# Optimization experiments

Hardware: AMD Instinct MI355X
Metric: run time of the kernel (lower is better)

Reference implementation:

```python
import jax, jax.numpy as jnp
import numpy as np

N_NODES = 50000
NEG_SLOPE = 0.2  # PyG GATConv leaky_relu default


def _gat_layer(x, src, dst, W, a_src, a_dst, bias, heads, ch):
    n = x.shape[0]
    h = (x @ W).reshape(n, heads, ch)                    # [N,H,C]
    alpha_s = jnp.sum(h * a_src, axis=-1)                # [N,H]
    alpha_d = jnp.sum(h * a_dst, axis=-1)                # [N,H]
    e = alpha_s[src] + alpha_d[dst]                      # [E,H]
    e = jnp.where(e > 0, e, NEG_SLOPE * e)               # leaky_relu
    # segment softmax over incoming edges of each dst node
    m = jax.ops.segment_max(e, dst, num_segments=n)      # [N,H]
    m = jnp.where(jnp.isfinite(m), m, 0.0)
    ex = jnp.exp(e - m[dst])                             # [E,H]
    denom = jax.ops.segment_sum(ex, dst, num_segments=n) # [N,H]
    alpha = ex / (denom[dst] + 1e-16)                    # [E,H]
    msg = alpha[:, :, None] * h[src]                     # [E,H,C]
    out = jax.ops.segment_sum(msg, dst, num_segments=n)  # [N,H,C]
    return out.reshape(n, heads * ch) + bias


def setup_inputs() -> dict:
    key = jax.random.key(0)
    ks = jax.random.split(key, 10)
    F_in, H1, C1, C2 = 256, 8, 32, 32
    E = 500000
    x = jax.random.normal(ks[0], (N_NODES, F_in), dtype=jnp.float32)
    edge_index = jax.random.randint(ks[1], (2, E), 0, N_NODES, dtype=jnp.int64)
    s1 = 1.0 / np.sqrt(F_in)
    s2 = 1.0 / np.sqrt(H1 * C1)
    return {
        "x": x,
        "edge_index": edge_index,
        "W1": jax.random.normal(ks[2], (F_in, H1 * C1), dtype=jnp.float32) * s1,
        "a_src1": jax.random.normal(ks[3], (H1, C1), dtype=jnp.float32) * s2,
        "a_dst1": jax.random.normal(ks[4], (H1, C1), dtype=jnp.float32) * s2,
        "b1": jnp.zeros((H1 * C1,), dtype=jnp.float32),
        "W2": jax.random.normal(ks[5], (H1 * C1, C2), dtype=jnp.float32) * s2,
        "a_src2": jax.random.normal(ks[6], (1, C2), dtype=jnp.float32) * (1.0 / np.sqrt(C2)),
        "a_dst2": jax.random.normal(ks[7], (1, C2), dtype=jnp.float32) * (1.0 / np.sqrt(C2)),
        "b2": jnp.zeros((C2,), dtype=jnp.float32),
    }


def reference(x, edge_index, W1, a_src1, a_dst1, b1, W2, a_src2, a_dst2, b2):
    n = x.shape[0]
    # add self-loops (PyG GATConv default add_self_loops=True)
    loop = jnp.arange(n, dtype=edge_index.dtype)
    src = jnp.concatenate([edge_index[0], loop])
    dst = jnp.concatenate([edge_index[1], loop])
    h = _gat_layer(x, src, dst, W1, a_src1, a_dst1, b1, heads=8, ch=32)
    h = jax.nn.elu(h)
    h = _gat_layer(h, src, dst, W2, a_src2, a_dst2, b2, heads=1, ch=32)
    return jax.nn.log_softmax(h, axis=1)
```

## Files before the change

### kernel.cpp

```cpp
#include <hip/hip_runtime.h>
#include <math.h>


typedef __attribute__((ext_vector_type(8))) short bf16x8;
typedef __attribute__((ext_vector_type(4))) float f32x4;

__device__ __forceinline__ float bf2f(ushort u) {
    union { uint i; float f; } v; v.i = ((uint)u) << 16; return v.f;
}
__device__ __forceinline__ ushort f2bf(float f) {
    union { float f; uint i; } v; v.f = f;
    uint r = v.i + 0x7FFFu + ((v.i >> 16) & 1u);
    return (ushort)(r >> 16);
}

__global__ void zero_kernel(int* p, int n) {
    int i = blockIdx.x * blockDim.x + threadIdx.x;
    if (i < n) p[i] = 0;
}

__global__ void detect_kernel(const int* ei32, int* flag) {
    __shared__ int cnt;
    if (threadIdx.x == 0) cnt = 0;
    __syncthreads();
    int nz = 0;
    for (int i = threadIdx.x; i < 1024; i += blockDim.x)
        if (ei32[2 * i + 1] != 0) nz++;
    atomicAdd(&cnt, nz);
    __syncthreads();
    if (threadIdx.x == 0) *flag = (cnt > 16) ? 1 : 0;
}

__global__ void decode_degree_kernel(const void* ei, int E, int ET, int N,
                                     const int* __restrict__ flag,
                                     int* __restrict__ src, int* __restrict__ dst,
                                     int* __restrict__ deg) {
    int k = blockIdx.x * blockDim.x + threadIdx.x;
    if (k >= ET) return;
    int s, d;
    if (k < E) {
        if (*flag) {
            const int* p = (const int*)ei;
            s = p[k]; d = p[E + k];
        } else {
            const long long* p = (const long long*)ei;
            s = (int)p[k]; d = (int)p[E + k];
        }
    } else {
        s = d = k - E;
    }
    s = min(max(s, 0), N - 1);
    d = min(max(d, 0), N - 1);
    src[k] = s; dst[k] = d;
    atomicAdd(&deg[d], 1);
}

__global__ __launch_bounds__(256) void scanA_kernel(const int* __restrict__ deg,
                                                    int* __restrict__ bsum, int n) {
    int i = blockIdx.x * 256 + threadIdx.x;
    int v = (i < n) ? deg[i] : 0;
#pragma unroll
    for (int s = 1; s < 64; s <<= 1) v += __shfl_xor(v, s, 64);
    __shared__ int ws[4];
    int lane = threadIdx.x & 63, wid = threadIdx.x >> 6;
    if (lane == 0) ws[wid] = v;
    __syncthreads();
    if (threadIdx.x == 0) bsum[blockIdx.x] = ws[0] + ws[1] + ws[2] + ws[3];
}

__global__ __launch_bounds__(1024) void scanB_kernel(int* __restrict__ bsum, int nb) {
    int t = threadIdx.x;
    int v = (t < nb) ? bsum[t] : 0;
    __shared__ int sm[1024];
    sm[t] = v;
    __syncthreads();
    for (int s = 1; s < 1024; s <<= 1) {
        int a = (t >= s) ? sm[t - s] : 0;
        __syncthreads();
        sm[t] += a;
        __syncthreads();
    }
    if (t < nb) bsum[t] = sm[t] - v;
}

__global__ __launch_bounds__(256) void scanC_kernel(const int* __restrict__ deg,
                                                    const int* __restrict__ bsum,
                                                    int* __restrict__ off, int n) {
    int t = threadIdx.x;
    int i = blockIdx.x * 256 + t;
    int v = (i < n) ? deg[i] : 0;
    int incl = v;
    int lane = t & 63, wid = t >> 6;
#pragma unroll
    for (int s = 1; s < 64; s <<= 1) {
        int a = __shfl_up(incl, s, 64);
        if (lane >= s) incl += a;
    }
    __shared__ int wsum[4];
    if (lane == 63) wsum[wid] = incl;
    __syncthreads();
    int wo = 0;
    for (int w = 0; w < wid; w++) wo += wsum[w];
    if (i < n) off[i + 1] = bsum[blockIdx.x] + wo + incl;
    if (i == 0) off[0] = 0;
}

__global__ void scatter_kernel(const int* __restrict__ src, const int* __restrict__ dst,
                               int ET, const int* __restrict__ off,
                               int* __restrict__ cursor, int* __restrict__ esrc) {
    int k = blockIdx.x * blockDim.x + threadIdx.x;
    if (k >= ET) return;
    int d = dst[k];
    int p = atomicAdd(&cursor[d], 1);
    esrc[off[d] + p] = src[k];
}

__global__ void convert_x(const float* __restrict__ x, ushort* __restrict__ xb, long n) {
    long i = ((long)blockIdx.x * blockDim.x + threadIdx.x) * 8;
    if (i >= n) return;
    float4 a = *(const float4*)&x[i];
    float4 b = *(const float4*)&x[i + 4];
    uint4 o;
    o.x = (uint)f2bf(a.x) | ((uint)f2bf(a.y) << 16);
    o.y = (uint)f2bf(a.z) | ((uint)f2bf(a.w) << 16);
    o.z = (uint)f2bf(b.x) | ((uint)f2bf(b.y) << 16);
    o.w = (uint)f2bf(b.z) | ((uint)f2bf(b.w) << 16);
    *(uint4*)&xb[i] = o;
}

__global__ __launch_bounds__(256) void convert_w1t(const float* __restrict__ W1,
                                                   ushort* __restrict__ w1t) {
    __shared__ float tile[32][33];
    int tx = threadIdx.x & 31, ty = threadIdx.x >> 5;
    int bx = blockIdx.x, by = blockIdx.y;
    for (int i = 0; i < 32; i += 8)
        tile[ty + i][tx] = W1[(by * 32 + ty + i) * 256 + bx * 32 + tx];
    __syncthreads();
    for (int i = 0; i < 32; i += 8)
        w1t[(bx * 32 + ty + i) * 256 + by * 32 + tx] = f2bf(tile[tx][ty + i]);
}

__global__ __launch_bounds__(256) void convert_w2t(const float* __restrict__ W2,
                                                   ushort* __restrict__ w2t) {
    int idx = blockIdx.x * 256 + threadIdx.x;
    int c = idx >> 8, k = idx & 255;
    w2t[idx] = f2bf(W2[k * 32 + c]);
}

#define LDA 72
__global__ __launch_bounds__(256) void gemm1_mfma(
        const ushort* __restrict__ xb,
        const ushort* __restrict__ w1t,
        ushort* __restrict__ h1b,
        int N) {
    __shared__ ushort Al[128 * LDA];
    __shared__ ushort Bl[128 * LDA];
    int t = threadIdx.x;
    int row0 = blockIdx.x * 128;
    int n0 = blockIdx.y * 128;
    int lane = t & 63, wid = t >> 6;
    int wr = wid >> 1, wc = wid & 1;

    f32x4 acc[4][4] = {};

    int sr = t >> 1, scs = (t & 1) * 32;
    for (int k0 = 0; k0 < 256; k0 += 64) {
        {
            int gr = row0 + sr;
            uint4 v0 = {0,0,0,0}, v1 = {0,0,0,0}, v2 = {0,0,0,0}, v3 = {0,0,0,0};
            if (gr < N) {
                const uint4* g = (const uint4*)(xb + (size_t)gr * 256 + k0 + scs);
                v0 = g[0]; v1 = g[1]; v2 = g[2]; v3 = g[3];
            }
            uint4* d = (uint4*)&Al[sr * LDA + scs];
            d[0] = v0; d[1] = v1; d[2] = v2; d[3] = v3;
        }
        {
            const uint4* g = (const uint4*)(w1t + (size_t)(n0 + sr) * 256 + k0 + scs);
            uint4* d = (uint4*)&Bl[sr * LDA + scs];
            d[0] = g[0]; d[1] = g[1]; d[2] = g[2]; d[3] = g[3];
        }
        __syncthreads();

#pragma unroll
        for (int ks = 0; ks < 2; ks++) {
            int kk = ks * 32 + (lane >> 4) * 8;
            bf16x8 af[4], bfr[4];
#pragma unroll
            for (int mi = 0; mi < 4; mi++) {
                int r = wr * 64 + mi * 16 + (lane & 15);
                af[mi] = *(const bf16x8*)&Al[r * LDA + kk];
            }
#pragma unroll
            for (int ni = 0; ni < 4; ni++) {
                int r = wc * 64 + ni * 16 + (lane & 15);
                bfr[ni] = *(const bf16x8*)&Bl[r * LDA + kk];
            }
#pragma unroll
            for (int mi = 0; mi < 4; mi++)
#pragma unroll
                for (int ni = 0; ni < 4; ni++)
                    acc[mi][ni] = __builtin_amdgcn_mfma_f32_16x16x32_bf16(
                        af[mi], bfr[ni], acc[mi][ni], 0, 0, 0);
        }
        __syncthreads();
    }

#pragma unroll
    for (int mi = 0; mi < 4; mi++)
#pragma unroll
        for (int ni = 0; ni < 4; ni++) {
            int gc = n0 + wc * 64 + ni * 16 + (lane & 15);
#pragma unroll
            for (int j = 0; j < 4; j++) {
                int gr = row0 + wr * 64 + mi * 16 + (lane >> 4) * 4 + j;
                if (gr < N) h1b[(size_t)gr * 256 + gc] = f2bf(acc[mi][ni][j]);
            }
        }
}

__global__ __launch_bounds__(256) void alpha1_kernel(
        const ushort* __restrict__ h1b,
        const float* __restrict__ a_src1, const float* __restrict__ a_dst1,
        float* __restrict__ as1, float* __restrict__ ad1, int N) {
    int t = threadIdx.x;
    int g = t >> 5, l = t & 31;
    int node = blockIdx.x * 8 + g;
    if (node >= N) return;
    bf16x8 hv = *(const bf16x8*)&h1b[(size_t)node * 256 + l * 8];
    float s = 0.f, d = 0.f;
#pragma unroll
    for (int i = 0; i < 8; i++) {
        float h = bf2f((ushort)hv[i]);
        s = fmaf(h, a_src1[l * 8 + i], s);
        d = fmaf(h, a_dst1[l * 8 + i], d);
    }
    s += __shfl_xor(s, 1); s += __shfl_xor(s, 2);
    d += __shfl_xor(d, 1); d += __shfl_xor(d, 2);
    if ((l & 3) == 0) {
        as1[node * 8 + (l >> 2)] = s;
        ad1[node * 8 + (l >> 2)] = d;
    }
}

__global__ __launch_bounds__(256) void weights1_kernel(
        const float* __restrict__ as1, const float* __restrict__ ad1,
        const int* __restrict__ off, const int* __restrict__ esrc,
        float* __restrict__ alf1, int NH) {
    int tid = blockIdx.x * 256 + threadIdx.x;
    if (tid >= NH) return;
    int node = tid >> 3, head = tid & 7;
    int beg = off[node], end = off[node + 1];
    float adv = ad1[tid];
    float m = -3.0e38f;
    for (int j = beg; j < end; j++) {
        float e = as1[esrc[j] * 8 + head] + adv;
        e = (e > 0.f) ? e : 0.2f * e;
        m = fmaxf(m, e);
    }
    float dnm = 0.f;
    for (int j = beg; j < end; j++) {
        float e = as1[esrc[j] * 8 + head] + adv;
        e = (e > 0.f) ? e : 0.2f * e;
        dnm += __expf(e - m);
    }
    float inv = 1.f / (dnm + 1e-16f);
    for (int j = beg; j < end; j++) {
        float e = as1[esrc[j] * 8 + head] + adv;
        e = (e > 0.f) ? e : 0.2f * e;
        alf1[(size_t)j * 8 + head] = __expf(e - m) * inv;
    }
}

__global__ __launch_bounds__(256) void agg1b_kernel(
        const ushort* __restrict__ h1b, const float* __restrict__ alf1,
        const float* __restrict__ b1,
        const int* __restrict__ off, const int* __restrict__ esrc,
        ushort* __restrict__ hactb, int N) {
    int t = threadIdx.x;
    int node = blockIdx.x * 4 + (t >> 6);
    int lane = t & 63;
    if (node >= N) return;
    int beg = off[node], end = off[node + 1];
    int ch0 = lane * 4;
    int head = lane >> 3;
    const ushort* hb = h1b + ch0;
    const float* af = alf1 + head;
    float c0 = 0.f, c1 = 0.f, c2 = 0.f, c3 = 0.f;
    int j = beg;
    for (; j + 4 <= end; j += 4) {
        int s0 = esrc[j + 0], s1 = esrc[j + 1], s2 = esrc[j + 2], s3 = esrc[j + 3];
        float w0 = af[(size_t)(j + 0) * 8];
        float w1 = af[(size_t)(j + 1) * 8];
        float w2 = af[(size_t)(j + 2) * 8];
        float w3 = af[(size_t)(j + 3) * 8];
        uint2 v0 = *(const uint2*)(hb + (size_t)s0 * 256);
        uint2 v1 = *(const uint2*)(hb + (size_t)s1 * 256);
        uint2 v2 = *(const uint2*)(hb + (size_t)s2 * 256);
        uint2 v3 = *(const uint2*)(hb + (size_t)s3 * 256);
        c0 = fmaf(w0, bf2f((ushort)(v0.x & 0xffffu)), c0);
        c1 = fmaf(w0, bf2f((ushort)(v0.x >> 16)), c1);
        c2 = fmaf(w0, bf2f((ushort)(v0.y & 0xffffu)), c2);
        c3 = fmaf(w0, bf2f((ushort)(v0.y >> 16)), c3);
        c0 = fmaf(w1, bf2f((ushort)(v1.x & 0xffffu)), c0);
        c1 = fmaf(w1, bf2f((ushort)(v1.x >> 16)), c1);
        c2 = fmaf(w1, bf2f((ushort)(v1.y & 0xffffu)), c2);
        c3 = fmaf(w1, bf2f((ushort)(v1.y >> 16)), c3);
        c0 = fmaf(w2, bf2f((ushort)(v2.x & 0xffffu)), c0);
        c1 = fmaf(w2, bf2f((ushort)(v2.x >> 16)), c1);
        c2 = fmaf(w2, bf2f((ushort)(v2.y & 0xffffu)), c2);
        c3 = fmaf(w2, bf2f((ushort)(v2.y >> 16)), c3);
        c0 = fmaf(w3, bf2f((ushort)(v3.x & 0xffffu)), c0);
        c1 = fmaf(w3, bf2f((ushort)(v3.x >> 16)), c1);
        c2 = fmaf(w3, bf2f((ushort)(v3.y & 0xffffu)), c2);
        c3 = fmaf(w3, bf2f((ushort)(v3.y >> 16)), c3);
    }
    for (; j < end; j++) {
        int s0 = esrc[j];
        float w = af[(size_t)j * 8];
        uint2 v = *(const uint2*)(hb + (size_t)s0 * 256);
        c0 = fmaf(w, bf2f((ushort)(v.x & 0xffffu)), c0);
        c1 = fmaf(w, bf2f((ushort)(v.x >> 16)), c1);
        c2 = fmaf(w, bf2f((ushort)(v.y & 0xffffu)), c2);
        c3 = fmaf(w, bf2f((ushort)(v.y >> 16)), c3);
    }
    float4 bv = *(const float4*)&b1[ch0];
    float o0 = c0 + bv.x, o1 = c1 + bv.y, o2 = c2 + bv.z, o3 = c3 + bv.w;
    o0 = (o0 > 0.f) ? o0 : (__expf(o0) - 1.f);
    o1 = (o1 > 0.f) ? o1 : (__expf(o1) - 1.f);
    o2 = (o2 > 0.f) ? o2 : (__expf(o2) - 1.f);
    o3 = (o3 > 0.f) ? o3 : (__expf(o3) - 1.f);
    uint2 r;
    r.x = (uint)f2bf(o0) | ((uint)f2bf(o1) << 16);
    r.y = (uint)f2bf(o2) | ((uint)f2bf(o3) << 16);
    *(uint2*)(hactb + (size_t)node * 256 + ch0) = r;
}

__global__ __launch_bounds__(256) void gemm2_mfma(
        const ushort* __restrict__ hactb,
        const ushort* __restrict__ w2t,
        float* __restrict__ h2, int N) {
    __shared__ ushort Al[128 * LDA];
    __shared__ ushort Bl[32 * LDA];
    int t = threadIdx.x;
    int row0 = blockIdx.x * 128;
    int lane = t & 63, wid = t >> 6;

    f32x4 acc[2][2] = {};

    int sr = t >> 1, scs = (t & 1) * 32;
    for (int k0 = 0; k0 < 256; k0 += 64) {
        {
            int gr = row0 + sr;
            uint4 v0 = {0,0,0,0}, v1 = {0,0,0,0}, v2 = {0,0,0,0}, v3 = {0,0,0,0};
            if (gr < N) {
                const uint4* g = (const uint4*)(hactb + (size_t)gr * 256 + k0 + scs);
                v0 = g[0]; v1 = g[1]; v2 = g[2]; v3 = g[3];
            }
            uint4* d = (uint4*)&Al[sr * LDA + scs];
            d[0] = v0; d[1] = v1; d[2] = v2; d[3] = v3;
        }
        if (t < 64) {
            const uint4* g = (const uint4*)(w2t + (size_t)sr * 256 + k0 + scs);
            uint4* d = (uint4*)&Bl[sr * LDA + scs];
            d[0] = g[0]; d[1] = g[1]; d[2] = g[2]; d[3] = g[3];
        }
        __syncthreads();

#pragma unroll
        for (int ks = 0; ks < 2; ks++) {
            int kk = ks * 32 + (lane >> 4) * 8;
            bf16x8 af[2], bfr[2];
#pragma unroll
            for (int mi = 0; mi < 2; mi++) {
                int r = wid * 32 + mi * 16 + (lane & 15);
                af[mi] = *(const bf16x8*)&Al[r * LDA + kk];
            }
#pragma unroll
            for (int ni = 0; ni < 2; ni++) {
                int r = ni * 16 + (lane & 15);
                bfr[ni] = *(const bf16x8*)&Bl[r * LDA + kk];
            }
#pragma unroll
            for (int mi = 0; mi < 2; mi++)
#pragma unroll
                for (int ni = 0; ni < 2; ni++)
                    acc[mi][ni] = __builtin_amdgcn_mfma_f32_16x16x32_bf16(
                        af[mi], bfr[ni], acc[mi][ni], 0, 0, 0);
        }
        __syncthreads();
    }

#pragma unroll
    for (int mi = 0; mi < 2; mi++)
#pragma unroll
        for (int ni = 0; ni < 2; ni++) {
            int gc = ni * 16 + (lane & 15);
#pragma unroll
            for (int j = 0; j < 4; j++) {
                int gr = row0 + wid * 32 + mi * 16 + (lane >> 4) * 4 + j;
                if (gr < N) h2[(size_t)gr * 32 + gc] = acc[mi][ni][j];
            }
        }
}

__global__ __launch_bounds__(256) void alpha2_kernel(
        const float* __restrict__ h2,
        const float* __restrict__ a_src2, const float* __restrict__ a_dst2,
        float* __restrict__ as2, float* __restrict__ ad2, int N) {
    int t = threadIdx.x;
    int g = t >> 3, q = t & 7;
    int node = blockIdx.x * 32 + g;
    if (node >= N) return;
    float4 v = *(const float4*)&h2[(size_t)node * 32 + q * 4];
    float4 sa = *(const float4*)&a_src2[q * 4];
    float4 da = *(const float4*)&a_dst2[q * 4];
    float s = v.x * sa.x + v.y * sa.y + v.z * sa.z + v.w * sa.w;
    float d = v.x * da.x + v.y * da.y + v.z * da.z + v.w * da.w;
    s += __shfl_xor(s, 1, 8); s += __shfl_xor(s, 2, 8); s += __shfl_xor(s, 4, 8);
    d += __shfl_xor(d, 1, 8); d += __shfl_xor(d, 2, 8); d += __shfl_xor(d, 4, 8);
    if (q == 0) { as2[node] = s; ad2[node] = d; }
}

__global__ __launch_bounds__(256) void weights2_kernel(
        const float* __restrict__ as2, const float* __restrict__ ad2,
        const int* __restrict__ off, const int* __restrict__ esrc,
        float* __restrict__ alf2, int N) {
    int t = threadIdx.x;
    int g = t >> 5, lane = t & 31;
    int node = blockIdx.x * 8 + g;
    if (node >= N) return;
    int beg = off[node], end = off[node + 1];
    float adv = ad2[node];
    float m = -3.0e38f, dnm = 0.f;
    for (int base = beg; base < end; base += 32) {
        int n_ch = min(32, end - base);
        float ej = -3.0e38f;
        if (lane < n_ch) {
            float e = as2[esrc[base + lane]] + adv;
            ej = (e > 0.f) ? e : 0.2f * e;
        }
        float cm = ej;
#pragma unroll
        for (int s = 16; s > 0; s >>= 1) cm = fmaxf(cm, __shfl_xor(cm, s, 32));
        float nm = fmaxf(m, cm);
        float scl = __expf(m - nm);
        float wj = (lane < n_ch) ? __expf(ej - nm) : 0.f;
        float ws = wj;
#pragma unroll
        for (int s = 16; s > 0; s >>= 1) ws += __shfl_xor(ws, s, 32);
        dnm = dnm * scl + ws;
        m = nm;
    }
    float inv = 1.f / (dnm + 1e-16f);
    for (int base = beg; base < end; base += 32) {
        int n_ch = min(32, end - base);
        if (lane < n_ch) {
            float e = as2[esrc[base + lane]] + adv;
            e = (e > 0.f) ? e : 0.2f * e;
            alf2[base + lane] = __expf(e - m) * inv;
        }
    }
}

__global__ __launch_bounds__(256) void agg2b_kernel(
        const float* __restrict__ h2, const float* __restrict__ alf2,
        const float* __restrict__ b2,
        const int* __restrict__ off, const int* __restrict__ esrc,
        float* __restrict__ out, int N) {
    int t = threadIdx.x;
    int g = t >> 5, c = t & 31;
    int node = blockIdx.x * 8 + g;
    if (node >= N) return;
    int beg = off[node], end = off[node + 1];
    const float* hcol = h2 + c;
    float a0 = 0.f, a1 = 0.f, a2 = 0.f, a3 = 0.f;
    int j = beg;
    for (; j + 4 <= end; j += 4) {
        int s0 = esrc[j + 0], s1 = esrc[j + 1], s2 = esrc[j + 2], s3 = esrc[j + 3];
        float w0 = alf2[j + 0], w1 = alf2[j + 1], w2 = alf2[j + 2], w3 = alf2[j + 3];
        a0 = fmaf(w0, hcol[(size_t)s0 * 32], a0);
        a1 = fmaf(w1, hcol[(size_t)s1 * 32], a1);
        a2 = fmaf(w2, hcol[(size_t)s2 * 32], a2);
        a3 = fmaf(w3, hcol[(size_t)s3 * 32], a3);
    }
    for (; j < end; j++)
        a0 = fmaf(alf2[j], hcol[(size_t)esrc[j] * 32], a0);
    float v = (a0 + a1) + (a2 + a3) + b2[c];
    float mx = v;
#pragma unroll
    for (int s = 16; s > 0; s >>= 1) mx = fmaxf(mx, __shfl_xor(mx, s, 32));
    float sum = __expf(v - mx);
#pragma unroll
    for (int s = 16; s > 0; s >>= 1) sum += __shfl_xor(sum, s, 32);
    out[(size_t)node * 32 + c] = (v - mx) - __logf(sum);
}

extern "C" void kernel_launch(void* const* d_in, const int* in_sizes, int n_in,
                              void* d_out, int out_size, void* d_ws, size_t ws_size,
                              hipStream_t stream) {
    const float* x      = (const float*)d_in[0];
    const void*  ei     = d_in[1];
    const float* W1     = (const float*)d_in[2];
    const float* a_src1 = (const float*)d_in[3];
    const float* a_dst1 = (const float*)d_in[4];
    const float* b1     = (const float*)d_in[5];
    const float* W2     = (const float*)d_in[6];
    const float* a_src2 = (const float*)d_in[7];
    const float* a_dst2 = (const float*)d_in[8];
    const float* b2     = (const float*)d_in[9];
    const int N  = in_sizes[0] / 256;
    const int E  = in_sizes[1] / 2;
    const int ET = E + N;
    float* outp = (float*)d_out;
    (void)n_in; (void)out_size; (void)ws_size;

    char* ws = (char*)d_ws;
    size_t o = 0;
    auto alloc = [&](size_t bytes) -> void* {
        void* p = ws + o;
        o += (bytes + 255) & ~(size_t)255;
        return p;
    };
    int*    flag   = (int*)alloc(4);
    int*    src32  = (int*)alloc((size_t)ET * 4);
    int*    dst32  = (int*)alloc((size_t)ET * 4);
    int*    deg    = (int*)alloc((size_t)2 * N * 4);
    int*    cursor = deg + N;
    int*    off    = (int*)alloc((size_t)(N + 1) * 4);
    int*    esrc   = (int*)alloc((size_t)ET * 4);
    int*    bsum   = (int*)alloc((size_t)1024 * 4);
    ushort* xb     = (ushort*)alloc((size_t)N * 256 * 2);
    ushort* w1t    = (ushort*)alloc((size_t)256 * 256 * 2);
    ushort* w2t    = (ushort*)alloc((size_t)32 * 256 * 2);
    ushort* h1b    = (ushort*)alloc((size_t)N * 256 * 2);
    float*  as1    = (float*)alloc((size_t)N * 8 * 4);
    float*  ad1    = (float*)alloc((size_t)N * 8 * 4);
    float*  alf1   = (float*)alloc((size_t)ET * 8 * 4);
    ushort* hactb  = (ushort*)alloc((size_t)N * 256 * 2);
    float*  h2     = (float*)alloc((size_t)N * 32 * 4);
    float*  as2    = (float*)alloc((size_t)N * 4);
    float*  ad2    = (float*)alloc((size_t)N * 4);
    float*  alf2   = (float*)alloc((size_t)ET * 4);

    const int nbScan = (N + 255) / 256;

    zero_kernel<<<(2 * N + 255) / 256, 256, 0, stream>>>(deg, 2 * N);
    detect_kernel<<<1, 256, 0, stream>>>((const int*)ei, flag);
    decode_degree_kernel<<<(ET + 255) / 256, 256, 0, stream>>>(ei, E, ET, N, flag,
                                                               src32, dst32, deg);
    scanA_kernel<<<nbScan, 256, 0, stream>>>(deg, bsum, N);
    scanB_kernel<<<1, 1024, 0, stream>>>(bsum, nbScan);
    scanC_kernel<<<nbScan, 256, 0, stream>>>(deg, bsum, off, N);
    scatter_kernel<<<(ET + 255) / 256, 256, 0, stream>>>(src32, dst32, ET, off,
                                                         cursor, esrc);

    long nx = (long)N * 256;
    convert_x<<<(int)((nx / 8 + 255) / 256), 256, 0, stream>>>(x, xb, nx);
    convert_w1t<<<dim3(8, 8), 256, 0, stream>>>(W1, w1t);
    convert_w2t<<<32, 256, 0, stream>>>(W2, w2t);

    gemm1_mfma<<<dim3((N + 127) / 128, 2), 256, 0, stream>>>(xb, w1t, h1b, N);
    alpha1_kernel<<<(N + 7) / 8, 256, 0, stream>>>(h1b, a_src1, a_dst1, as1, ad1, N);
    weights1_kernel<<<(N * 8 + 255) / 256, 256, 0, stream>>>(as1, ad1, off, esrc,
                                                             alf1, N * 8);
    agg1b_kernel<<<(N + 3) / 4, 256, 0, stream>>>(h1b, alf1, b1, off, esrc, hactb, N);
    gemm2_mfma<<<(N + 127) / 128, 256, 0, stream>>>(hactb, w2t, h2, N);
    alpha2_kernel<<<(N + 31) / 32, 256, 0, stream>>>(h2, a_src2, a_dst2, as2, ad2, N);
    weights2_kernel<<<(N + 7) / 8, 256, 0, stream>>>(as2, ad2, off, esrc, alf2, N);
    agg2b_kernel<<<(N + 7) / 8, 256, 0, stream>>>(h2, alf2, b2, off, esrc, outp, N);
}
```

Measured before the change: 225.0 us.

## Fuse x bf16 conversion into GEMM1 load and batch agg1 gathers by eight

Removes the separate convert_x pass and its bf16 staging buffer. gemm1 now reads fp32 x directly and packs it to bf16 while filling shared memory, which saves one full write and read of an N×256 array. Because the grid has two column blocks, each x row is now read twice in fp32, which adds some read traffic. The layer-1 aggregation loop also issues eight predicated gathers at a time to raise memory-level parallelism, at the cost of wasted work in tail iterations.

```diff
diff --git a/kernel.cpp b/kernel.cpp
--- a/kernel.cpp
+++ b/kernel.cpp
@@ -12,6 +12,9 @@
     union { float f; uint i; } v; v.f = f;
     uint r = v.i + 0x7FFFu + ((v.i >> 16) & 1u);
     return (ushort)(r >> 16);
+}
+__device__ __forceinline__ uint pack2(float a, float b) {
+    return (uint)f2bf(a) | ((uint)f2bf(b) << 16);
 }
 
 __global__ void zero_kernel(int* p, int n) {
@@ -115,19 +118,6 @@
     esrc[off[d] + p] = src[k];
 }
 
-__global__ void convert_x(const float* __restrict__ x, ushort* __restrict__ xb, long n) {
-    long i = ((long)blockIdx.x * blockDim.x + threadIdx.x) * 8;
-    if (i >= n) return;
-    float4 a = *(const float4*)&x[i];
-    float4 b = *(const float4*)&x[i + 4];
-    uint4 o;
-    o.x = (uint)f2bf(a.x) | ((uint)f2bf(a.y) << 16);
-    o.y = (uint)f2bf(a.z) | ((uint)f2bf(a.w) << 16);
-    o.z = (uint)f2bf(b.x) | ((uint)f2bf(b.y) << 16);
-    o.w = (uint)f2bf(b.z) | ((uint)f2bf(b.w) << 16);
-    *(uint4*)&xb[i] = o;
-}
-
 __global__ __launch_bounds__(256) void convert_w1t(const float* __restrict__ W1,
                                                    ushort* __restrict__ w1t) {
     __shared__ float tile[32][33];
@@ -149,7 +139,7 @@
 
 #define LDA 72
 __global__ __launch_bounds__(256) void gemm1_mfma(
-        const ushort* __restrict__ xb,
+        const float* __restrict__ x,
         const ushort* __restrict__ w1t,
         ushort* __restrict__ h1b,
         int N) {
@@ -167,13 +157,25 @@
     for (int k0 = 0; k0 < 256; k0 += 64) {
         {
             int gr = row0 + sr;
-            uint4 v0 = {0,0,0,0}, v1 = {0,0,0,0}, v2 = {0,0,0,0}, v3 = {0,0,0,0};
+            float4 f[8];
             if (gr < N) {
-                const uint4* g = (const uint4*)(xb + (size_t)gr * 256 + k0 + scs);
-                v0 = g[0]; v1 = g[1]; v2 = g[2]; v3 = g[3];
+                const float4* g = (const float4*)(x + (size_t)gr * 256 + k0 + scs);
+#pragma unroll
+                for (int q = 0; q < 8; q++) f[q] = g[q];
+            } else {
+#pragma unroll
+                for (int q = 0; q < 8; q++) f[q] = float4{0.f, 0.f, 0.f, 0.f};
             }
             uint4* d = (uint4*)&Al[sr * LDA + scs];
-            d[0] = v0; d[1] = v1; d[2] = v2; d[3] = v3;
+#pragma unroll
+            for (int p = 0; p < 4; p++) {
+                uint4 u;
+                u.x = pack2(f[2 * p].x, f[2 * p].y);
+                u.y = pack2(f[2 * p].z, f[2 * p].w);
+                u.z = pack2(f[2 * p + 1].x, f[2 * p + 1].y);
+                u.w = pack2(f[2 * p + 1].z, f[2 * p + 1].w);
+                d[p] = u;
+            }
         }
         {
             const uint4* g = (const uint4*)(w1t + (size_t)(n0 + sr) * 256 + k0 + scs);
@@ -287,42 +289,25 @@
     const ushort* hb = h1b + ch0;
     const float* af = alf1 + head;
     float c0 = 0.f, c1 = 0.f, c2 = 0.f, c3 = 0.f;
-    int j = beg;
-    for (; j + 4 <= end; j += 4) {
-        int s0 = esrc[j + 0], s1 = esrc[j + 1], s2 = esrc[j + 2], s3 = esrc[j + 3];
-        float w0 = af[(size_t)(j + 0) * 8];
-        float w1 = af[(size_t)(j + 1) * 8];
-        float w2 = af[(size_t)(j + 2) * 8];
-        float w3 = af[(size_t)(j + 3) * 8];
-        uint2 v0 = *(const uint2*)(hb + (size_t)s0 * 256);
-        uint2 v1 = *(const uint2*)(hb + (size_t)s1 * 256);
-        uint2 v2 = *(const uint2*)(hb + (size_t)s2 * 256);
-        uint2 v3 = *(const uint2*)(hb + (size_t)s3 * 256);
-        c0 = fmaf(w0, bf2f((ushort)(v0.x & 0xffffu)), c0);
-        c1 = fmaf(w0, bf2f((ushort)(v0.x >> 16)), c1);
-        c2 = fmaf(w0, bf2f((ushort)(v0.y & 0xffffu)), c2);
-        c3 = fmaf(w0, bf2f((ushort)(v0.y >> 16)), c3);
-        c0 = fmaf(w1, bf2f((ushort)(v1.x & 0xffffu)), c0);
-        c1 = fmaf(w1, bf2f((ushort)(v1.x >> 16)), c1);
-        c2 = fmaf(w1, bf2f((ushort)(v1.y & 0xffffu)), c2);
-        c3 = fmaf(w1, bf2f((ushort)(v1.y >> 16)), c3);
-        c0 = fmaf(w2, bf2f((ushort)(v2.x & 0xffffu)), c0);
-        c1 = fmaf(w2, bf2f((ushort)(v2.x >> 16)), c1);
-        c2 = fmaf(w2, bf2f((ushort)(v2.y & 0xffffu)), c2);
-        c3 = fmaf(w2, bf2f((ushort)(v2.y >> 16)), c3);
-        c0 = fmaf(w3, bf2f((ushort)(v3.x & 0xffffu)), c0);
-        c1 = fmaf(w3, bf2f((ushort)(v3.x >> 16)), c1);
-        c2 = fmaf(w3, bf2f((ushort)(v3.y & 0xffffu)), c2);
-        c3 = fmaf(w3, bf2f((ushort)(v3.y >> 16)), c3);
-    }
-    for (; j < end; j++) {
-        int s0 = esrc[j];
-        float w = af[(size_t)j * 8];
-        uint2 v = *(const uint2*)(hb + (size_t)s0 * 256);
-        c0 = fmaf(w, bf2f((ushort)(v.x & 0xffffu)), c0);
-        c1 = fmaf(w, bf2f((ushort)(v.x >> 16)), c1);
-        c2 = fmaf(w, bf2f((ushort)(v.y & 0xffffu)), c2);
-        c3 = fmaf(w, bf2f((ushort)(v.y >> 16)), c3);
+    for (int j0 = beg; j0 < end; j0 += 8) {
+        int ss[8]; float ww[8]; uint2 vv[8];
+#pragma unroll
+        for (int q = 0; q < 8; q++) {
+            int j = j0 + q;
+            bool ok = (j < end);
+            ss[q] = ok ? esrc[j] : 0;
+            ww[q] = ok ? af[(size_t)j * 8] : 0.f;
+        }
+#pragma unroll
+        for (int q = 0; q < 8; q++)
+            vv[q] = *(const uint2*)(hb + (size_t)ss[q] * 256);
+#pragma unroll
+        for (int q = 0; q < 8; q++) {
+            c0 = fmaf(ww[q], bf2f((ushort)(vv[q].x & 0xffffu)), c0);
+            c1 = fmaf(ww[q], bf2f((ushort)(vv[q].x >> 16)), c1);
+            c2 = fmaf(ww[q], bf2f((ushort)(vv[q].y & 0xffffu)), c2);
+            c3 = fmaf(ww[q], bf2f((ushort)(vv[q].y >> 16)), c3);
+        }
     }
     float4 bv = *(const float4*)&b1[ch0];
     float o0 = c0 + bv.x, o1 = c1 + bv.y, o2 = c2 + bv.z, o3 = c3 + bv.w;
@@ -530,7 +515,6 @@
     int*    off    = (int*)alloc((size_t)(N + 1) * 4);
     int*    esrc   = (int*)alloc((size_t)ET * 4);
     int*    bsum   = (int*)alloc((size_t)1024 * 4);
-    ushort* xb     = (ushort*)alloc((size_t)N * 256 * 2);
     ushort* w1t    = (ushort*)alloc((size_t)256 * 256 * 2);
     ushort* w2t    = (ushort*)alloc((size_t)32 * 256 * 2);
     ushort* h1b    = (ushort*)alloc((size_t)N * 256 * 2);
@@ -555,12 +539,10 @@
     scatter_kernel<<<(ET + 255) / 256, 256, 0, stream>>>(src32, dst32, ET, off,
                                                          cursor, esrc);
 
-    long nx = (long)N * 256;
-    convert_x<<<(int)((nx / 8 + 255) / 256), 256, 0, stream>>>(x, xb, nx);
     convert_w1t<<<dim3(8, 8), 256, 0, stream>>>(W1, w1t);
     convert_w2t<<<32, 256, 0, stream>>>(W2, w2t);
 
-    gemm1_mfma<<<dim3((N + 127) / 128, 2), 256, 0, stream>>>(xb, w1t, h1b, N);
+    gemm1_mfma<<<dim3((N + 127) / 128, 2), 256, 0, stream>>>(x, w1t, h1b, N);
     alpha1_kernel<<<(N + 7) / 8, 256, 0, stream>>>(h1b, a_src1, a_dst1, as1, ad1, N);
     weights1_kernel<<<(N * 8 + 255) / 256, 256, 0, stream>>>(as1, ad1, off, esrc,
                                                              alf1, N * 8);
```

After: 231.7 us. +3.0%, slower.

## Fuse softmax weights into aggregation kernels and bf16 conversion into GEMM load

Applied to the files above, without the earlier changes.

Folds the per-edge softmax weight computation for both GAT layers into the aggregation kernels, recomputing attention logits on the fly instead of writing and rereading alf1/alf2 edge arrays. Converts x from fp32 to bf16 inside the GEMM1 tile load, removing the separate convert_x pass and its intermediate buffer. Replaces the zero kernel with hipMemsetAsync. The trade-off is extra gathers of as1/as2 and exp work per edge, plus doubled fp32 global reads of x in GEMM1 because each row is loaded by both column blocks.

```diff
diff --git a/kernel.cpp b/kernel.cpp
--- a/kernel.cpp
+++ b/kernel.cpp
@@ -13,10 +13,8 @@
     uint r = v.i + 0x7FFFu + ((v.i >> 16) & 1u);
     return (ushort)(r >> 16);
 }
-
-__global__ void zero_kernel(int* p, int n) {
-    int i = blockIdx.x * blockDim.x + threadIdx.x;
-    if (i < n) p[i] = 0;
+__device__ __forceinline__ uint pack2(float a, float b) {
+    return (uint)f2bf(a) | ((uint)f2bf(b) << 16);
 }
 
 __global__ void detect_kernel(const int* ei32, int* flag) {
@@ -115,19 +113,6 @@
     esrc[off[d] + p] = src[k];
 }
 
-__global__ void convert_x(const float* __restrict__ x, ushort* __restrict__ xb, long n) {
-    long i = ((long)blockIdx.x * blockDim.x + threadIdx.x) * 8;
-    if (i >= n) return;
-    float4 a = *(const float4*)&x[i];
-    float4 b = *(const float4*)&x[i + 4];
-    uint4 o;
-    o.x = (uint)f2bf(a.x) | ((uint)f2bf(a.y) << 16);
-    o.y = (uint)f2bf(a.z) | ((uint)f2bf(a.w) << 16);
-    o.z = (uint)f2bf(b.x) | ((uint)f2bf(b.y) << 16);
-    o.w = (uint)f2bf(b.z) | ((uint)f2bf(b.w) << 16);
-    *(uint4*)&xb[i] = o;
-}
-
 __global__ __launch_bounds__(256) void convert_w1t(const float* __restrict__ W1,
                                                    ushort* __restrict__ w1t) {
     __shared__ float tile[32][33];
@@ -149,7 +134,7 @@
 
 #define LDA 72
 __global__ __launch_bounds__(256) void gemm1_mfma(
-        const ushort* __restrict__ xb,
+        const float* __restrict__ x,
         const ushort* __restrict__ w1t,
         ushort* __restrict__ h1b,
         int N) {
@@ -167,13 +152,25 @@
     for (int k0 = 0; k0 < 256; k0 += 64) {
         {
             int gr = row0 + sr;
-            uint4 v0 = {0,0,0,0}, v1 = {0,0,0,0}, v2 = {0,0,0,0}, v3 = {0,0,0,0};
+            float4 f[8];
             if (gr < N) {
-                const uint4* g = (const uint4*)(xb + (size_t)gr * 256 + k0 + scs);
-                v0 = g[0]; v1 = g[1]; v2 = g[2]; v3 = g[3];
+                const float4* g = (const float4*)(x + (size_t)gr * 256 + k0 + scs);
+#pragma unroll
+                for (int q = 0; q < 8; q++) f[q] = g[q];
+            } else {
+#pragma unroll
+                for (int q = 0; q < 8; q++) f[q] = float4{0.f, 0.f, 0.f, 0.f};
             }
             uint4* d = (uint4*)&Al[sr * LDA + scs];
-            d[0] = v0; d[1] = v1; d[2] = v2; d[3] = v3;
+#pragma unroll
+            for (int p = 0; p < 4; p++) {
+                uint4 u;
+                u.x = pack2(f[2 * p].x, f[2 * p].y);
+                u.y = pack2(f[2 * p].z, f[2 * p].w);
+                u.z = pack2(f[2 * p + 1].x, f[2 * p + 1].y);
+                u.w = pack2(f[2 * p + 1].z, f[2 * p + 1].w);
+                d[p] = u;
+            }
         }
         {
             const uint4* g = (const uint4*)(w1t + (size_t)(n0 + sr) * 256 + k0 + scs);
@@ -243,37 +240,9 @@
     }
 }
 
-__global__ __launch_bounds__(256) void weights1_kernel(
+__global__ __launch_bounds__(256) void agg1c_kernel(
+        const ushort* __restrict__ h1b,
         const float* __restrict__ as1, const float* __restrict__ ad1,
-        const int* __restrict__ off, const int* __restrict__ esrc,
-        float* __restrict__ alf1, int NH) {
-    int tid = blockIdx.x * 256 + threadIdx.x;
-    if (tid >= NH) return;
-    int node = tid >> 3, head = tid & 7;
-    int beg = off[node], end = off[node + 1];
-    float adv = ad1[tid];
-    float m = -3.0e38f;
-    for (int j = beg; j < end; j++) {
-        float e = as1[esrc[j] * 8 + head] + adv;
-        e = (e > 0.f) ? e : 0.2f * e;
-        m = fmaxf(m, e);
-    }
-    float dnm = 0.f;
-    for (int j = beg; j < end; j++) {
-        float e = as1[esrc[j] * 8 + head] + adv;
-        e = (e > 0.f) ? e : 0.2f * e;
-        dnm += __expf(e - m);
-    }
-    float inv = 1.f / (dnm + 1e-16f);
-    for (int j = beg; j < end; j++) {
-        float e = as1[esrc[j] * 8 + head] + adv;
-        e = (e > 0.f) ? e : 0.2f * e;
-        alf1[(size_t)j * 8 + head] = __expf(e - m) * inv;
-    }
-}
-
-__global__ __launch_bounds__(256) void agg1b_kernel(
-        const ushort* __restrict__ h1b, const float* __restrict__ alf1,
         const float* __restrict__ b1,
         const int* __restrict__ off, const int* __restrict__ esrc,
         ushort* __restrict__ hactb, int N) {
@@ -282,18 +251,58 @@
     int lane = t & 63;
     if (node >= N) return;
     int beg = off[node], end = off[node + 1];
+
+    int h = lane & 7, q = lane >> 3;
+    float adv = ad1[node * 8 + h];
+    float m = -3.0e38f;
+    for (int j0 = beg; j0 < end; j0 += 8) {
+        int j = j0 + q;
+        if (j < end) {
+            float e = as1[esrc[j] * 8 + h] + adv;
+            e = (e > 0.f) ? e : 0.2f * e;
+            m = fmaxf(m, e);
+        }
+    }
+    m = fmaxf(m, __shfl_xor(m, 8));
+    m = fmaxf(m, __shfl_xor(m, 16));
+    m = fmaxf(m, __shfl_xor(m, 32));
+    float dnm = 0.f;
+    for (int j0 = beg; j0 < end; j0 += 8) {
+        int j = j0 + q;
+        if (j < end) {
+            float e = as1[esrc[j] * 8 + h] + adv;
+            e = (e > 0.f) ? e : 0.2f * e;
+            dnm += __expf(e - m);
+        }
+    }
+    dnm += __shfl_xor(dnm, 8);
+    dnm += __shfl_xor(dnm, 16);
+    dnm += __shfl_xor(dnm, 32);
+    float inv = 1.f / (dnm + 1e-16f);
+
+    int head2 = lane >> 3;
+    float m2   = __shfl(m, head2);
+    float inv2 = __shfl(inv, head2);
+    float adv2 = __shfl(adv, head2);
     int ch0 = lane * 4;
-    int head = lane >> 3;
     const ushort* hb = h1b + ch0;
-    const float* af = alf1 + head;
+    const float* asp = as1 + head2;
     float c0 = 0.f, c1 = 0.f, c2 = 0.f, c3 = 0.f;
     int j = beg;
     for (; j + 4 <= end; j += 4) {
         int s0 = esrc[j + 0], s1 = esrc[j + 1], s2 = esrc[j + 2], s3 = esrc[j + 3];
-        float w0 = af[(size_t)(j + 0) * 8];
-        float w1 = af[(size_t)(j + 1) * 8];
-        float w2 = af[(size_t)(j + 2) * 8];
-        float w3 = af[(size_t)(j + 3) * 8];
+        float e0 = asp[s0 * 8] + adv2;
+        float e1 = asp[s1 * 8] + adv2;
+        float e2 = asp[s2 * 8] + adv2;
+        float e3 = asp[s3 * 8] + adv2;
+        e0 = (e0 > 0.f) ? e0 : 0.2f * e0;
+        e1 = (e1 > 0.f) ? e1 : 0.2f * e1;
+        e2 = (e2 > 0.f) ? e2 : 0.2f * e2;
+        e3 = (e3 > 0.f) ? e3 : 0.2f * e3;
+        float w0 = __expf(e0 - m2) * inv2;
+        float w1 = __expf(e1 - m2) * inv2;
+        float w2 = __expf(e2 - m2) * inv2;
+        float w3 = __expf(e3 - m2) * inv2;
         uint2 v0 = *(const uint2*)(hb + (size_t)s0 * 256);
         uint2 v1 = *(const uint2*)(hb + (size_t)s1 * 256);
         uint2 v2 = *(const uint2*)(hb + (size_t)s2 * 256);
@@ -317,7 +326,9 @@
     }
     for (; j < end; j++) {
         int s0 = esrc[j];
-        float w = af[(size_t)j * 8];
+        float e = asp[s0 * 8] + adv2;
+        e = (e > 0.f) ? e : 0.2f * e;
+        float w = __expf(e - m2) * inv2;
         uint2 v = *(const uint2*)(hb + (size_t)s0 * 256);
         c0 = fmaf(w, bf2f((ushort)(v.x & 0xffffu)), c0);
         c1 = fmaf(w, bf2f((ushort)(v.x >> 16)), c1);
@@ -422,22 +433,25 @@
     if (q == 0) { as2[node] = s; ad2[node] = d; }
 }
 
-__global__ __launch_bounds__(256) void weights2_kernel(
+__global__ __launch_bounds__(256) void agg2c_kernel(
+        const float* __restrict__ h2,
         const float* __restrict__ as2, const float* __restrict__ ad2,
+        const float* __restrict__ b2,
         const int* __restrict__ off, const int* __restrict__ esrc,
-        float* __restrict__ alf2, int N) {
-    int t = threadIdx.x;
-    int g = t >> 5, lane = t & 31;
+        float* __restrict__ out, int N) {
+    int t = threadIdx.x;
+    int g = t >> 5, c = t & 31;
     int node = blockIdx.x * 8 + g;
     if (node >= N) return;
     int beg = off[node], end = off[node + 1];
     float adv = ad2[node];
+
     float m = -3.0e38f, dnm = 0.f;
     for (int base = beg; base < end; base += 32) {
         int n_ch = min(32, end - base);
         float ej = -3.0e38f;
-        if (lane < n_ch) {
-            float e = as2[esrc[base + lane]] + adv;
+        if (c < n_ch) {
+            float e = as2[esrc[base + c]] + adv;
             ej = (e > 0.f) ? e : 0.2f * e;
         }
         float cm = ej;
@@ -445,7 +459,7 @@
         for (int s = 16; s > 0; s >>= 1) cm = fmaxf(cm, __shfl_xor(cm, s, 32));
         float nm = fmaxf(m, cm);
         float scl = __expf(m - nm);
-        float wj = (lane < n_ch) ? __expf(ej - nm) : 0.f;
+        float wj = (c < n_ch) ? __expf(ej - nm) : 0.f;
         float ws = wj;
 #pragma unroll
         for (int s = 16; s > 0; s >>= 1) ws += __shfl_xor(ws, s, 32);
@@ -453,39 +467,31 @@
         m = nm;
     }
     float inv = 1.f / (dnm + 1e-16f);
-    for (int base = beg; base < end; base += 32) {
-        int n_ch = min(32, end - base);
-        if (lane < n_ch) {
-            float e = as2[esrc[base + lane]] + adv;
-            e = (e > 0.f) ? e : 0.2f * e;
-            alf2[base + lane] = __expf(e - m) * inv;
-        }
-    }
-}
-
-__global__ __launch_bounds__(256) void agg2b_kernel(
-        const float* __restrict__ h2, const float* __restrict__ alf2,
-        const float* __restrict__ b2,
-        const int* __restrict__ off, const int* __restrict__ esrc,
-        float* __restrict__ out, int N) {
-    int t = threadIdx.x;
-    int g = t >> 5, c = t & 31;
-    int node = blockIdx.x * 8 + g;
-    if (node >= N) return;
-    int beg = off[node], end = off[node + 1];
+
     const float* hcol = h2 + c;
     float a0 = 0.f, a1 = 0.f, a2 = 0.f, a3 = 0.f;
     int j = beg;
     for (; j + 4 <= end; j += 4) {
         int s0 = esrc[j + 0], s1 = esrc[j + 1], s2 = esrc[j + 2], s3 = esrc[j + 3];
-        float w0 = alf2[j + 0], w1 = alf2[j + 1], w2 = alf2[j + 2], w3 = alf2[j + 3];
+        float e0 = as2[s0] + adv, e1 = as2[s1] + adv;
+        float e2 = as2[s2] + adv, e3 = as2[s3] + adv;
+        e0 = (e0 > 0.f) ? e0 : 0.2f * e0;
+        e1 = (e1 > 0.f) ? e1 : 0.2f * e1;
+        e2 = (e2 > 0.f) ? e2 : 0.2f * e2;
+        e3 = (e3 > 0.f) ? e3 : 0.2f * e3;
+        float w0 = __expf(e0 - m) * inv, w1 = __expf(e1 - m) * inv;
+        float w2 = __expf(e2 - m) * inv, w3 = __expf(e3 - m) * inv;
         a0 = fmaf(w0, hcol[(size_t)s0 * 32], a0);
         a1 = fmaf(w1, hcol[(size_t)s1 * 32], a1);
         a2 = fmaf(w2, hcol[(size_t)s2 * 32], a2);
         a3 = fmaf(w3, hcol[(size_t)s3 * 32], a3);
     }
-    for (; j < end; j++)
-        a0 = fmaf(alf2[j], hcol[(size_t)esrc[j] * 32], a0);
+    for (; j < end; j++) {
+        int s0 = esrc[j];
+        float e = as2[s0] + adv;
+        e = (e > 0.f) ? e : 0.2f * e;
+        a0 = fmaf(__expf(e - m) * inv, hcol[(size_t)s0 * 32], a0);
+    }
     float v = (a0 + a1) + (a2 + a3) + b2[c];
     float mx = v;
 #pragma unroll
@@ -530,22 +536,19 @@
     int*    off    = (int*)alloc((size_t)(N + 1) * 4);
     int*    esrc   = (int*)alloc((size_t)ET * 4);
     int*    bsum   = (int*)alloc((size_t)1024 * 4);
-    ushort* xb     = (ushort*)alloc((size_t)N * 256 * 2);
     ushort* w1t    = (ushort*)alloc((size_t)256 * 256 * 2);
     ushort* w2t    = (ushort*)alloc((size_t)32 * 256 * 2);
     ushort* h1b    = (ushort*)alloc((size_t)N * 256 * 2);
     float*  as1    = (float*)alloc((size_t)N * 8 * 4);
     float*  ad1    = (float*)alloc((size_t)N * 8 * 4);
-    float*  alf1   = (float*)alloc((size_t)ET * 8 * 4);
     ushort* hactb  = (ushort*)alloc((size_t)N * 256 * 2);
     float*  h2     = (float*)alloc((size_t)N * 32 * 4);
     float*  as2    = (float*)alloc((size_t)N * 4);
     float*  ad2    = (float*)alloc((size_t)N * 4);
-    float*  alf2   = (float*)alloc((size_t)ET * 4);
 
     const int nbScan = (N + 255) / 256;
 
-    zero_kernel<<<(2 * N + 255) / 256, 256, 0, stream>>>(deg, 2 * N);
+    hipMemsetAsync(deg, 0, (size_t)2 * N * 4, stream);
     detect_kernel<<<1, 256, 0, stream>>>((const int*)ei, flag);
     decode_degree_kernel<<<(ET + 255) / 256, 256, 0, stream>>>(ei, E, ET, N, flag,
                                                                src32, dst32, deg);
@@ -555,18 +558,15 @@
     scatter_kernel<<<(ET + 255) / 256, 256, 0, stream>>>(src32, dst32, ET, off,
                                                          cursor, esrc);
 
-    long nx = (long)N * 256;
-    convert_x<<<(int)((nx / 8 + 255) / 256), 256, 0, stream>>>(x, xb, nx);
     convert_w1t<<<dim3(8, 8), 256, 0, stream>>>(W1, w1t);
     convert_w2t<<<32, 256, 0, stream>>>(W2, w2t);
 
-    gemm1_mfma<<<dim3((N + 127) / 128, 2), 256, 0, stream>>>(xb, w1t, h1b, N);
+    gemm1_mfma<<<dim3((N + 127) / 128, 2), 256, 0, stream>>>(x, w1t, h1b, N);
     alpha1_kernel<<<(N + 7) / 8, 256, 0, stream>>>(h1b, a_src1, a_dst1, as1, ad1, N);
-    weights1_kernel<<<(N * 8 + 255) / 256, 256, 0, stream>>>(as1, ad1, off, esrc,
-                                                             alf1, N * 8);
-    agg1b_kernel<<<(N + 3) / 4, 256, 0, stream>>>(h1b, alf1, b1, off, esrc, hactb, N);
+    agg1c_kernel<<<(N + 3) / 4, 256, 0, stream>>>(h1b, as1, ad1, b1, off, esrc,
+                                                  hactb, N);
     gemm2_mfma<<<(N + 127) / 128, 256, 0, stream>>>(hactb, w2t, h2, N);
     alpha2_kernel<<<(N + 31) / 32, 256, 0, stream>>>(h2, a_src2, a_dst2, as2, ad2, N);
-    weights2_kernel<<<(N + 7) / 8, 256, 0, stream>>>(as2, ad2, off, esrc, alf2, N);
-    agg2b_kernel<<<(N + 7) / 8, 256, 0, stream>>>(h2, alf2, b2, off, esrc, outp, N);
-}
+    agg2c_kernel<<<(N + 7) / 8, 256, 0, stream>>>(h2, as2, ad2, b2, off, esrc,
+                                                  outp, N);
+}
```

New measurement: 209.5 us. 1.07x faster.
